# Optimization experiments

Measured on AMD Instinct MI355X. Metric: run time of the kernel, lower is better.

## Reference

```python
import jax, jax.numpy as jnp
import numpy as np

B, N, NP, NS = 8, 4096, 1024, 32
CF = 64            # input point-feature channels; in_channel = 3 + CF = 67
MLP = [64, 128, 256]
EPS = 1e-5         # BatchNorm eps (torch default)


def setup_inputs() -> dict:
    key = jax.random.key(0)
    ks = jax.random.split(key, 8)
    inp = {
        "xyz": jax.random.normal(ks[0], (B, N, 3), jnp.float32),
        "points": jax.random.normal(ks[1], (B, CF, N), jnp.float32),
        "sample_idx": jax.random.randint(ks[2], (B, NP), 0, N, dtype=jnp.int32),
        "neighbor_idx": jax.random.randint(ks[3], (B, NP, NS), 0, N, dtype=jnp.int32),
    }
    c = 3 + CF
    for i, o in enumerate(MLP):
        wk = jax.random.fold_in(ks[4], i)
        inp[f"W{i}"] = jax.random.normal(wk, (o, c), jnp.float32) * (1.0 / np.sqrt(c))
        inp[f"b{i}"] = jnp.zeros((o,), jnp.float32)
        inp[f"gamma{i}"] = jnp.ones((o,), jnp.float32)
        inp[f"beta{i}"] = jnp.zeros((o,), jnp.float32)
        c = o
    return inp


def _forward(xyz, points, sample_idx, neighbor_idx, params):
    # xyz: (B,N,3)  points: (B,CF,N)
    new_xyz = jnp.take_along_axis(xyz, sample_idx[:, :, None], axis=1)        # (B,NP,3)
    nbr_xyz = jax.vmap(lambda x, idx: x[idx])(xyz, neighbor_idx)               # (B,NP,NS,3)
    rel = nbr_xyz - new_xyz[:, :, None, :]                                     # (B,NP,NS,3)
    nbr_feat = jax.vmap(lambda f, idx: f[:, idx])(points, neighbor_idx)        # (B,CF,NP,NS)
    x = jnp.concatenate([rel.transpose(0, 3, 1, 2), nbr_feat], axis=1)         # (B,3+CF,NP,NS)
    # 1x1 Conv2d -> BatchNorm2d (training-mode batch stats) -> ReLU stack
    for W, b, g, be in params:
        x = jnp.einsum('oc,bcps->bops', W, x) + b[None, :, None, None]
        mu = x.mean(axis=(0, 2, 3), keepdims=True)
        var = x.var(axis=(0, 2, 3), keepdims=True)
        x = g[None, :, None, None] * (x - mu) * jax.lax.rsqrt(var + EPS) + be[None, :, None, None]
        x = jax.nn.relu(x)
    new_points = x.max(axis=-1)                                                # (B,C_out,NP)
    return new_xyz, new_points


def reference(xyz, points, sample_idx, neighbor_idx,
              W0, b0, gamma0, beta0,
              W1, b1, gamma1, beta1,
              W2, b2, gamma2, beta2):
    params = [(W0, b0, gamma0, beta0), (W1, b1, gamma1, beta1), (W2, b2, gamma2, beta2)]
    return _forward(xyz, points, sample_idx, neighbor_idx, params)
```

## Files before the change

### kernel.cpp

```cpp
#include <hip/hip_runtime.h>

typedef unsigned short u16;
typedef unsigned int u32;
typedef __attribute__((ext_vector_type(8))) short short8;
typedef __attribute__((ext_vector_type(16))) float f32x16;

#define BB 8
#define NN 4096
#define NPP 1024
#define NSS 32
#define CFF 64
#define C0 67
#define H0 64
#define H1 128
#define H2 256
#define MTOT (BB*NPP*NSS)
#define BN_EPS 1e-5f
#define INV_M (1.0f/262144.0f)

#define MFMA32(a,b,c) __builtin_amdgcn_mfma_f32_32x32x16_bf16(a,b,c,0,0,0)

__device__ __forceinline__ float bf2f(u16 h){ return __uint_as_float(((u32)h)<<16); }
__device__ __forceinline__ u16 f2bf(float f){
  u32 u = __float_as_uint(f);
  u32 r = (u + 0x7fffu + ((u>>16)&1u)) >> 16;
  return (u16)r;
}
__device__ __forceinline__ u32 pack2(float a, float b){
  return (u32)f2bf(a) | ((u32)f2bf(b)<<16);
}

#define WS_NEED 46280704u

__global__ __launch_bounds__(256) void k_setup(
    const float* __restrict__ xyz, const float* __restrict__ points,
    const int* __restrict__ sidx,
    const float* __restrict__ W0, const float* __restrict__ W1, const float* __restrict__ W2,
    u16* __restrict__ ptsT, u16* __restrict__ Wt0c, u16* __restrict__ Wt1c,
    u16* __restrict__ Wt2c, float* __restrict__ out_newxyz, float* __restrict__ stats)
{
  int blk = blockIdx.x, tid = threadIdx.x;
  if (blk < 512) {
    __shared__ float t[64][68];
    int b = blk >> 6, n0 = (blk & 63) << 6;
    for (int it = 0; it < 4; ++it) {
      int u = it*256 + tid;
      int nq = u & 15, c = u >> 4;
      float4 v = *(const float4*)&points[(size_t)(b*CFF + c)*NN + n0 + nq*4];
      *(float4*)&t[c][nq*4] = v;
    }
    __syncthreads();
    for (int it = 0; it < 2; ++it) {
      int u = it*256 + tid;
      int oct = u & 7, n = u >> 3;
      u16 pk[8];
#pragma unroll
      for (int j = 0; j < 8; ++j) pk[j] = f2bf(t[oct*8 + j][n]);
      *(uint4*)&ptsT[((size_t)(b*NN + n0 + n))*CFF + oct*8] = *(uint4*)pk;
    }
  } else if (blk < 544) {
    int t0 = (blk - 512)*256 + tid;
    int b = t0 >> 10;
    int s = sidx[t0];
    for (int k = 0; k < 3; ++k)
      out_newxyz[(size_t)t0*3 + k] = xyz[((size_t)(b*NN + s))*3 + k];
  } else if (blk == 544) {
    for (int i = 0; i < 24; ++i) {
      int e = i*256 + tid;
      int kc = e >> 9, o = (e >> 3) & 63, j = e & 7, k = kc*8 + j;
      float v = (k < 64) ? W0[o*C0 + 3 + k] : ((k < 67) ? W0[o*C0 + (k - 64)] : 0.f);
      Wt0c[e] = f2bf(v);
    }
  } else if (blk == 545) {
    for (int i = 0; i < 32; ++i) {
      int e = i*256 + tid;
      int kc = e >> 10, n = (e >> 3) & 127, j = e & 7;
      Wt1c[e] = f2bf(W1[n*H0 + kc*8 + j]);
    }
  } else if (blk == 554) {
    float4 z = {0.f, 0.f, 0.f, 0.f};
    float4* p = (float4*)stats;
#pragma unroll
    for (int i = 0; i < 12; ++i) p[i*256 + tid] = z;
  } else {
    int base = (blk - 546) * 4096;
    for (int i = 0; i < 16; ++i) {
      int e = base + i*256 + tid;
      int kc = e >> 11, n = (e >> 3) & 255, j = e & 7;
      Wt2c[e] = f2bf(W2[n*H1 + kc*8 + j]);
    }
  }
}

__global__ __launch_bounds__(256) void k_xyz_only(
    const float* __restrict__ xyz, const int* __restrict__ sidx, float* __restrict__ out_newxyz)
{
  int t0 = blockIdx.x*256 + threadIdx.x;
  int b = t0 >> 10;
  int s = sidx[t0];
  for (int k = 0; k < 3; ++k)
    out_newxyz[(size_t)t0*3 + k] = xyz[((size_t)(b*NN + s))*3 + k];
}

__global__ __launch_bounds__(256) void k_l0(
    const float* __restrict__ xyz, const int* __restrict__ sidx, const int* __restrict__ nidx,
    const u16* __restrict__ ptsT, const u16* __restrict__ Wt0c,
    u16* __restrict__ y0, float* __restrict__ stats)
{
  __shared__ u16 XLc[12*128*8];
  __shared__ u16 W0c[12*64*8];
  int tid = threadIdx.x;
  int m0 = blockIdx.x * 128;
  int b = m0 >> 15;

  for (int i = 0; i < 3; ++i)
    ((uint4*)W0c)[i*256 + tid] = ((const uint4*)Wt0c)[i*256 + tid];

  int pos = tid & 127, half = tid >> 7;
  int m = m0 + pos;
  int nb = nidx[m];
  {
    const uint4* prow = (const uint4*)(ptsT + ((size_t)(b*NN + nb))*CFF + half*32);
    uint4 h0 = prow[0], h1 = prow[1], h2 = prow[2], h3 = prow[3];
    *(uint4*)&XLc[((half*4+0)*128 + pos)*8] = h0;
    *(uint4*)&XLc[((half*4+1)*128 + pos)*8] = h1;
    *(uint4*)&XLc[((half*4+2)*128 + pos)*8] = h2;
    *(uint4*)&XLc[((half*4+3)*128 + pos)*8] = h3;
    if (half == 0) {
      int p = (m & 32767) >> 5;
      int sp = sidx[b*NPP + p];
      float r0 = xyz[((size_t)(b*NN+nb))*3+0] - xyz[((size_t)(b*NN+sp))*3+0];
      float r1 = xyz[((size_t)(b*NN+nb))*3+1] - xyz[((size_t)(b*NN+sp))*3+1];
      float r2 = xyz[((size_t)(b*NN+nb))*3+2] - xyz[((size_t)(b*NN+sp))*3+2];
      uint4 v = { pack2(r0, r1), pack2(r2, 0.f), 0u, 0u };
      *(uint4*)&XLc[(8*128 + pos)*8] = v;
    } else {
      uint4 z = {0u,0u,0u,0u};
      *(uint4*)&XLc[(9*128 + pos)*8]  = z;
      *(uint4*)&XLc[(10*128 + pos)*8] = z;
      *(uint4*)&XLc[(11*128 + pos)*8] = z;
    }
  }
  __syncthreads();

  int lane = tid & 63, wv = tid >> 6;
  int l31 = lane & 31, kh = lane >> 5;
  int nt = wv & 1, mtb = (wv >> 1) * 2;
  f32x16 acc[2];
  for (int mi = 0; mi < 2; ++mi) for (int r = 0; r < 16; ++r) acc[mi][r] = 0.f;

  for (int kt = 0; kt < 6; ++kt) {
    int ck = kt*2 + kh;
    short8 bfrag = *(const short8*)&W0c[(ck*64 + nt*32 + l31)*8];
    for (int mi = 0; mi < 2; ++mi) {
      short8 afrag = *(const short8*)&XLc[(ck*128 + (mtb+mi)*32 + l31)*8];
      acc[mi] = MFMA32(afrag, bfrag, acc[mi]);
    }
  }

  float s = 0.f, q = 0.f;
  for (int mi = 0; mi < 2; ++mi)
    for (int r = 0; r < 16; ++r) { float y = acc[mi][r]; s += y; q += y*y; }
  s += __shfl_xor(s, 32); q += __shfl_xor(q, 32);
  if (lane < 32) {
    int slot = blockIdx.x & 7;
    atomicAdd(&stats[slot*256 + nt*32 + lane], s);
    atomicAdd(&stats[2048 + slot*256 + nt*32 + lane], q);
  }

  __syncthreads();
  {
    int chx = (nt*32 + l31) ^ (kh*32);
#pragma unroll
    for (int mi = 0; mi < 2; ++mi)
#pragma unroll
      for (int r = 0; r < 16; ++r) {
        int mm = (mtb+mi)*32 + (r&3) + 8*(r>>2) + 4*kh;
        XLc[mm*64 + chx] = f2bf(acc[mi][r]);
      }
  }
  __syncthreads();
  {
    uint4* dst = (uint4*)(y0 + (size_t)m0*H0);
#pragma unroll
    for (int i = 0; i < 4; ++i) {
      int t16 = i*256 + tid;
      int mrow = t16 >> 3, ch0 = (t16 & 7)*8;
      int idx = mrow*64 + (ch0 ^ (32*((mrow>>2)&1)));
      dst[t16] = *(const uint4*)&XLc[idx];
    }
  }
}

__global__ __launch_bounds__(256, 4) void k_l1s(
    const u16* __restrict__ y0, const u16* __restrict__ Wt1c,
    const float* __restrict__ g0, const float* __restrict__ e0,
    const float* __restrict__ stIn, float* __restrict__ stOut)
{
  __shared__ u16 X0c[8*128*8];
  __shared__ float scl0[64], sft0[64];
  int tid = threadIdx.x;
  int m0 = blockIdx.x * 128;
  int lane = tid & 63, wv = tid >> 6;
  int l31 = lane & 31, kh = lane >> 5;

  int pos = tid & 127, half = tid >> 7;
  u16 hs[32];
  {
    const u16* row = y0 + (size_t)(m0 + pos)*H0 + half*32;
#pragma unroll
    for (int t = 0; t < 4; ++t) *(uint4*)&hs[t*8] = ((const uint4*)row)[t];
  }
  short8 b1[4];
#pragma unroll
  for (int kt = 0; kt < 4; ++kt)
    b1[kt] = *(const short8*)&Wt1c[((kt*2 + kh)*128 + wv*32 + l31)*8];

  if (tid < 64) {
    float s = 0.f, q = 0.f;
    for (int sl = 0; sl < 8; ++sl) { s += stIn[sl*256 + tid]; q += stIn[2048 + sl*256 + tid]; }
    float mu = s*INV_M, var = q*INV_M - mu*mu;
    float sc = g0[tid] * rsqrtf(var + BN_EPS);
    scl0[tid] = sc; sft0[tid] = e0[tid] - mu*sc;
  }
  __syncthreads();

  {
    u16 ob[32];
#pragma unroll
    for (int j = 0; j < 32; ++j) {
      int c = half*32 + j;
      ob[j] = f2bf(fmaxf(fmaf(scl0[c], bf2f(hs[j]), sft0[c]), 0.f));
    }
#pragma unroll
    for (int t = 0; t < 4; ++t)
      *(uint4*)&X0c[((half*4+t)*128 + pos)*8] = *(uint4*)&ob[t*8];
  }
  __syncthreads();

  f32x16 acc[4];
#pragma unroll
  for (int mt = 0; mt < 4; ++mt) for (int r = 0; r < 16; ++r) acc[mt][r] = 0.f;

#pragma unroll
  for (int kt = 0; kt < 4; ++kt) {
    int ck = kt*2 + kh;
#pragma unroll
    for (int mt = 0; mt < 4; ++mt) {
      short8 afrag = *(const short8*)&X0c[(ck*128 + mt*32 + l31)*8];
      acc[mt] = MFMA32(afrag, b1[kt], acc[mt]);
    }
  }

  float s = 0.f, q = 0.f;
#pragma unroll
  for (int mt = 0; mt < 4; ++mt)
#pragma unroll
    for (int r = 0; r < 16; ++r) { float y = acc[mt][r]; s += y; q += y*y; }
  s += __shfl_xor(s, 32); q += __shfl_xor(q, 32);
  if (lane < 32) {
    int slot = blockIdx.x & 7;
    atomicAdd(&stOut[slot*256 + wv*32 + lane], s);
    atomicAdd(&stOut[2048 + slot*256 + wv*32 + lane], q);
  }
}

__global__ __launch_bounds__(256, 4) void k_l2f(
    const u16* __restrict__ y0, const u16* __restrict__ Wt1c, const u16* __restrict__ Wt2c,
    const float* __restrict__ g0, const float* __restrict__ e0,
    const float* __restrict__ g1, const float* __restrict__ e1,
    const float* __restrict__ st0, const float* __restrict__ st1, float* __restrict__ stOut,
    u16* __restrict__ mxp, u16* __restrict__ mnp)
{
  __shared__ u16 X0c[8*64*8];
  __shared__ u16 X1c[16*64*8];
  __shared__ float scl0[64], sft0[64], scl1[128], sft1[128];
  int tid = threadIdx.x;
  int m0 = blockIdx.x * 64;
  int lane = tid & 63, wv = tid >> 6;
  int l31 = lane & 31, kh = lane >> 5;

  int pos = tid & 63, grp = tid >> 6;
  u16 hs[16];
  {
    const u16* row = y0 + (size_t)(m0 + pos)*H0 + grp*16;
    *(uint4*)&hs[0] = ((const uint4*)row)[0];
    *(uint4*)&hs[8] = ((const uint4*)row)[1];
  }
  short8 b1[4];
#pragma unroll
  for (int kt = 0; kt < 4; ++kt)
    b1[kt] = *(const short8*)&Wt1c[((kt*2 + kh)*128 + wv*32 + l31)*8];

  if (tid < 64) {
    float s = 0.f, q = 0.f;
    for (int sl = 0; sl < 8; ++sl) { s += st0[sl*256 + tid]; q += st0[2048 + sl*256 + tid]; }
    float mu = s*INV_M, var = q*INV_M - mu*mu;
    float sc = g0[tid] * rsqrtf(var + BN_EPS);
    scl0[tid] = sc; sft0[tid] = e0[tid] - mu*sc;
  }
  if (tid < 128) {
    float s = 0.f, q = 0.f;
    for (int sl = 0; sl < 8; ++sl) { s += st1[sl*256 + tid]; q += st1[2048 + sl*256 + tid]; }
    float mu = s*INV_M, var = q*INV_M - mu*mu;
    float sc = g1[tid] * rsqrtf(var + BN_EPS);
    scl1[tid] = sc; sft1[tid] = e1[tid] - mu*sc;
  }
  __syncthreads();

  {
    u16 ob[16];
#pragma unroll
    for (int j = 0; j < 16; ++j) {
      int c = grp*16 + j;
      ob[j] = f2bf(fmaxf(fmaf(scl0[c], bf2f(hs[j]), sft0[c]), 0.f));
    }
    *(uint4*)&X0c[((2*grp)*64 + pos)*8]   = *(uint4*)&ob[0];
    *(uint4*)&X0c[((2*grp+1)*64 + pos)*8] = *(uint4*)&ob[8];
  }
  __syncthreads();

  f32x16 acc1[2];
#pragma unroll
  for (int mt = 0; mt < 2; ++mt) for (int r = 0; r < 16; ++r) acc1[mt][r] = 0.f;
#pragma unroll
  for (int kt = 0; kt < 4; ++kt) {
    int ck = kt*2 + kh;
#pragma unroll
    for (int mt = 0; mt < 2; ++mt) {
      short8 afrag = *(const short8*)&X0c[(ck*64 + mt*32 + l31)*8];
      acc1[mt] = MFMA32(afrag, b1[kt], acc1[mt]);
    }
  }

  {
    int ch1 = wv*32 + l31;
    int cb = ch1 >> 3, cr = ch1 & 7, sw = cb & 3;
    float sc1 = scl1[ch1], sf1 = sft1[ch1];
#pragma unroll
    for (int mt = 0; mt < 2; ++mt)
#pragma unroll
      for (int r = 0; r < 16; ++r) {
        int mm = mt*32 + (r&3) + 8*(r>>2) + 4*kh;
        X1c[(cb*64 + (mm ^ sw))*8 + cr] = f2bf(fmaxf(fmaf(sc1, acc1[mt][r], sf1), 0.f));
      }
  }
  __syncthreads();

  f32x16 acc2[2][2];
#pragma unroll
  for (int nt = 0; nt < 2; ++nt) for (int mt = 0; mt < 2; ++mt)
    for (int r = 0; r < 16; ++r) acc2[nt][mt][r] = 0.f;

#pragma unroll
  for (int k4 = 0; k4 < 8; ++k4) {
    int ck = k4*2 + kh;
    int sw = ck & 3;
    short8 bf_[2];
#pragma unroll
    for (int nt = 0; nt < 2; ++nt)
      bf_[nt] = *(const short8*)&Wt2c[(ck*256 + wv*64 + nt*32 + l31)*8];
    short8 a[2];
#pragma unroll
    for (int mt = 0; mt < 2; ++mt)
      a[mt] = *(const short8*)&X1c[(ck*64 + ((mt*32 + l31) ^ sw))*8];
#pragma unroll
    for (int nt = 0; nt < 2; ++nt)
#pragma unroll
      for (int mt = 0; mt < 2; ++mt)
        acc2[nt][mt] = MFMA32(a[mt], bf_[nt], acc2[nt][mt]);
  }

  int slot = blockIdx.x & 7;
#pragma unroll
  for (int nt = 0; nt < 2; ++nt) {
    float s = 0.f, q = 0.f;
    float mx[2] = {-3.0e38f, -3.0e38f}, mn[2] = {3.0e38f, 3.0e38f};
#pragma unroll
    for (int mt = 0; mt < 2; ++mt)
#pragma unroll
      for (int r = 0; r < 16; ++r) {
        float y = acc2[nt][mt][r];
        s += y; q += y*y;
        mx[mt] = fmaxf(mx[mt], y); mn[mt] = fminf(mn[mt], y);
      }
    s += __shfl_xor(s, 32); q += __shfl_xor(q, 32);
    mx[0] = fmaxf(mx[0], __shfl_xor(mx[0], 32));
    mx[1] = fmaxf(mx[1], __shfl_xor(mx[1], 32));
    mn[0] = fminf(mn[0], __shfl_xor(mn[0], 32));
    mn[1] = fminf(mn[1], __shfl_xor(mn[1], 32));
    if (lane < 32) {
      int c = wv*64 + nt*32 + lane;
      atomicAdd(&stOut[slot*256 + c], s);
      atomicAdd(&stOut[2048 + slot*256 + c], q);
#pragma unroll
      for (int mt = 0; mt < 2; ++mt) {
        size_t pr = (size_t)blockIdx.x*2 + mt;
        mxp[pr*H2 + c] = f2bf(mx[mt]);
        mnp[pr*H2 + c] = f2bf(mn[mt]);
      }
    }
  }
}

__global__ __launch_bounds__(256) void k_final(
    const u16* __restrict__ mxp, const u16* __restrict__ mnp,
    const float* __restrict__ gma, const float* __restrict__ bta,
    const float* __restrict__ stIn, float* __restrict__ out_np)
{
  __shared__ float tmp[256][33];
  int tid = threadIdx.x;
  int b = blockIdx.x >> 5;
  int p0 = (blockIdx.x & 31) * 32;

  float s = 0.f, q = 0.f;
  for (int sl = 0; sl < 8; ++sl) { s += stIn[sl*256 + tid]; q += stIn[2048 + sl*256 + tid]; }
  float mu = s*INV_M, var = q*INV_M - mu*mu;
  float sc = gma[tid] * rsqrtf(var + BN_EPS);
  float sh = bta[tid] - mu*sc;

  for (int pp = 0; pp < 32; ++pp) {
    size_t base = ((size_t)(b*NPP + p0 + pp))*H2 + tid;
    float xv = bf2f(mxp[base]), nv = bf2f(mnp[base]);
    float v = (sc >= 0.f) ? fmaf(sc, xv, sh) : fmaf(sc, nv, sh);
    tmp[tid][pp] = fmaxf(v, 0.f);
  }
  __syncthreads();

  int pl = tid & 31, cg = tid >> 5;
  for (int cc = 0; cc < 32; ++cc) {
    int c = cc*8 + cg;
    out_np[((size_t)b*H2 + c)*NPP + p0 + pl] = tmp[c][pl];
  }
}

extern "C" void kernel_launch(void* const* d_in, const int* in_sizes, int n_in,
                              void* d_out, int out_size, void* d_ws, size_t ws_size,
                              hipStream_t stream)
{
  const float* xyz    = (const float*)d_in[0];
  const float* points = (const float*)d_in[1];
  const int*   sidx   = (const int*)d_in[2];
  const int*   nidx   = (const int*)d_in[3];
  const float* W0 = (const float*)d_in[4];
  const float* g0 = (const float*)d_in[6];
  const float* e0 = (const float*)d_in[7];
  const float* W1 = (const float*)d_in[8];
  const float* g1 = (const float*)d_in[10];
  const float* e1 = (const float*)d_in[11];
  const float* W2 = (const float*)d_in[12];
  const float* g2 = (const float*)d_in[14];
  const float* e2 = (const float*)d_in[15];

  float* out_xyz = (float*)d_out;
  float* out_np  = out_xyz + (size_t)BB*NPP*3;

  if (ws_size < (size_t)WS_NEED) {
    hipMemsetAsync(out_np, 0, (size_t)BB*H2*NPP*4, stream);
    k_xyz_only<<<32, 256, 0, stream>>>(xyz, sidx, out_xyz);
    return;
  }

  char* ws = (char*)d_ws;
  float* stats = (float*)(ws + 0);
  u16*   Wt0c  = (u16*)(ws + 49152);
  u16*   Wt1c  = (u16*)(ws + 61440);
  u16*   Wt2c  = (u16*)(ws + 77824);
  u16*   ptsT  = (u16*)(ws + 143360);
  u16*   y0    = (u16*)(ws + 4337664);
  u16*   mxp   = (u16*)(ws + 37892096);
  u16*   mnp   = (u16*)(ws + 42086400);

  k_setup<<<555, 256, 0, stream>>>(xyz, points, sidx, W0, W1, W2,
                                   ptsT, Wt0c, Wt1c, Wt2c, out_xyz, stats);
  k_l0<<<MTOT/128, 256, 0, stream>>>(xyz, sidx, nidx, ptsT, Wt0c, y0, stats);
  k_l1s<<<MTOT/128, 256, 0, stream>>>(y0, Wt1c, g0, e0, stats, stats + 4096);
  k_l2f<<<MTOT/64, 256, 0, stream>>>(y0, Wt1c, Wt2c, g0, e0, g1, e1,
                                     stats, stats + 4096, stats + 8192, mxp, mnp);
  k_final<<<256, 256, 0, stream>>>(mxp, mnp, g2, e2, stats + 8192, out_np);
}
```

Before: 166.8 us.

## Fuse all stages into one persistent kernel with software grid barriers

Replaces the five separate launches (setup, layer0, layer1 stats, layer2 fused, final) with a single persistent kernel of 512 blocks that loops over tiles and uses atomic-counter grid barriers between phases. A tiny init kernel clears the barrier counters. This removes per-launch overhead and inter-kernel gaps. The risk is that it relies on all 512 blocks being co-resident, that the barriers' spinning and fences add cost, and that the fixed grid may lower occupancy compared with launching thousands of blocks per stage.

```diff
diff --git a/kernel.cpp b/kernel.cpp
--- a/kernel.cpp
+++ b/kernel.cpp
@@ -17,6 +17,7 @@
 #define MTOT (BB*NPP*NSS)
 #define BN_EPS 1e-5f
 #define INV_M (1.0f/262144.0f)
+#define NBLK 512
 
 #define MFMA32(a,b,c) __builtin_amdgcn_mfma_f32_32x32x16_bf16(a,b,c,0,0,0)
 
@@ -30,66 +31,30 @@
   return (u32)f2bf(a) | ((u32)f2bf(b)<<16);
 }
 
-#define WS_NEED 46280704u
-
-__global__ __launch_bounds__(256) void k_setup(
-    const float* __restrict__ xyz, const float* __restrict__ points,
-    const int* __restrict__ sidx,
-    const float* __restrict__ W0, const float* __restrict__ W1, const float* __restrict__ W2,
-    u16* __restrict__ ptsT, u16* __restrict__ Wt0c, u16* __restrict__ Wt1c,
-    u16* __restrict__ Wt2c, float* __restrict__ out_newxyz, float* __restrict__ stats)
+#define WS_NEED 46281728u
+
+__device__ __forceinline__ void gbar(char* bar, int idx) {
+  __syncthreads();
+  if (threadIdx.x == 0) {
+    __threadfence();
+    int* cnt = (int*)(bar + idx*256);
+    int* gen = (int*)(bar + idx*256 + 128);
+    if (__hip_atomic_fetch_add(cnt, 1, __ATOMIC_ACQ_REL, __HIP_MEMORY_SCOPE_AGENT) == NBLK - 1) {
+      __hip_atomic_store(gen, 1, __ATOMIC_RELEASE, __HIP_MEMORY_SCOPE_AGENT);
+    } else {
+      int spins = 0;
+      while (__hip_atomic_load(gen, __ATOMIC_ACQUIRE, __HIP_MEMORY_SCOPE_AGENT) == 0) {
+        if (++spins > (1 << 24)) break;
+      }
+    }
+    __threadfence();
+  }
+  __syncthreads();
+}
+
+__global__ __launch_bounds__(256) void k_binit(char* __restrict__ bar)
 {
-  int blk = blockIdx.x, tid = threadIdx.x;
-  if (blk < 512) {
-    __shared__ float t[64][68];
-    int b = blk >> 6, n0 = (blk & 63) << 6;
-    for (int it = 0; it < 4; ++it) {
-      int u = it*256 + tid;
-      int nq = u & 15, c = u >> 4;
-      float4 v = *(const float4*)&points[(size_t)(b*CFF + c)*NN + n0 + nq*4];
-      *(float4*)&t[c][nq*4] = v;
-    }
-    __syncthreads();
-    for (int it = 0; it < 2; ++it) {
-      int u = it*256 + tid;
-      int oct = u & 7, n = u >> 3;
-      u16 pk[8];
-#pragma unroll
-      for (int j = 0; j < 8; ++j) pk[j] = f2bf(t[oct*8 + j][n]);
-      *(uint4*)&ptsT[((size_t)(b*NN + n0 + n))*CFF + oct*8] = *(uint4*)pk;
-    }
-  } else if (blk < 544) {
-    int t0 = (blk - 512)*256 + tid;
-    int b = t0 >> 10;
-    int s = sidx[t0];
-    for (int k = 0; k < 3; ++k)
-      out_newxyz[(size_t)t0*3 + k] = xyz[((size_t)(b*NN + s))*3 + k];
-  } else if (blk == 544) {
-    for (int i = 0; i < 24; ++i) {
-      int e = i*256 + tid;
-      int kc = e >> 9, o = (e >> 3) & 63, j = e & 7, k = kc*8 + j;
-      float v = (k < 64) ? W0[o*C0 + 3 + k] : ((k < 67) ? W0[o*C0 + (k - 64)] : 0.f);
-      Wt0c[e] = f2bf(v);
-    }
-  } else if (blk == 545) {
-    for (int i = 0; i < 32; ++i) {
-      int e = i*256 + tid;
-      int kc = e >> 10, n = (e >> 3) & 127, j = e & 7;
-      Wt1c[e] = f2bf(W1[n*H0 + kc*8 + j]);
-    }
-  } else if (blk == 554) {
-    float4 z = {0.f, 0.f, 0.f, 0.f};
-    float4* p = (float4*)stats;
-#pragma unroll
-    for (int i = 0; i < 12; ++i) p[i*256 + tid] = z;
-  } else {
-    int base = (blk - 546) * 4096;
-    for (int i = 0; i < 16; ++i) {
-      int e = base + i*256 + tid;
-      int kc = e >> 11, n = (e >> 3) & 255, j = e & 7;
-      Wt2c[e] = f2bf(W2[n*H1 + kc*8 + j]);
-    }
-  }
+  if (threadIdx.x < 256) ((int*)bar)[threadIdx.x] = 0;
 }
 
 __global__ __launch_bounds__(256) void k_xyz_only(
@@ -102,335 +67,406 @@
     out_newxyz[(size_t)t0*3 + k] = xyz[((size_t)(b*NN + s))*3 + k];
 }
 
-__global__ __launch_bounds__(256) void k_l0(
-    const float* __restrict__ xyz, const int* __restrict__ sidx, const int* __restrict__ nidx,
-    const u16* __restrict__ ptsT, const u16* __restrict__ Wt0c,
-    u16* __restrict__ y0, float* __restrict__ stats)
+__global__ __launch_bounds__(256, 4) void k_all(
+    const float* __restrict__ xyz, const float* __restrict__ points,
+    const int* __restrict__ sidx, const int* __restrict__ nidx,
+    const float* __restrict__ W0, const float* __restrict__ g0, const float* __restrict__ e0,
+    const float* __restrict__ W1, const float* __restrict__ g1, const float* __restrict__ e1,
+    const float* __restrict__ W2, const float* __restrict__ g2, const float* __restrict__ e2,
+    char* __restrict__ ws, float* __restrict__ out_xyz)
 {
-  __shared__ u16 XLc[12*128*8];
-  __shared__ u16 W0c[12*64*8];
-  int tid = threadIdx.x;
-  int m0 = blockIdx.x * 128;
-  int b = m0 >> 15;
-
-  for (int i = 0; i < 3; ++i)
-    ((uint4*)W0c)[i*256 + tid] = ((const uint4*)Wt0c)[i*256 + tid];
-
-  int pos = tid & 127, half = tid >> 7;
-  int m = m0 + pos;
-  int nb = nidx[m];
+  __shared__ __align__(16) unsigned char smem[36864];
+  float* stats = (float*)ws;
+  u16* Wt0c = (u16*)(ws + 49152);
+  u16* Wt1c = (u16*)(ws + 61440);
+  u16* Wt2c = (u16*)(ws + 77824);
+  u16* ptsT = (u16*)(ws + 143360);
+  u16* y0   = (u16*)(ws + 4337664);
+  u16* mxp  = (u16*)(ws + 37892096);
+  u16* mnp  = (u16*)(ws + 42086400);
+  char* bar = ws + 46280704;
+  float* out_np = out_xyz + (size_t)BB*NPP*3;
+
+  int bid = blockIdx.x, tid = threadIdx.x;
+
+  for (int u = bid; u < 555; u += NBLK) {
+    if (u < 512) {
+      float (*t)[68] = (float(*)[68])smem;
+      int b = u >> 6, n0 = (u & 63) << 6;
+      for (int it = 0; it < 4; ++it) {
+        int e = it*256 + tid;
+        int nq = e & 15, c = e >> 4;
+        float4 v = *(const float4*)&points[(size_t)(b*CFF + c)*NN + n0 + nq*4];
+        *(float4*)&t[c][nq*4] = v;
+      }
+      __syncthreads();
+      for (int it = 0; it < 2; ++it) {
+        int e = it*256 + tid;
+        int oct = e & 7, n = e >> 3;
+        u16 pk[8];
+#pragma unroll
+        for (int j = 0; j < 8; ++j) pk[j] = f2bf(t[oct*8 + j][n]);
+        *(uint4*)&ptsT[((size_t)(b*NN + n0 + n))*CFF + oct*8] = *(uint4*)pk;
+      }
+      __syncthreads();
+    } else if (u < 544) {
+      int t0 = (u - 512)*256 + tid;
+      int b = t0 >> 10;
+      int s = sidx[t0];
+      for (int k = 0; k < 3; ++k)
+        out_xyz[(size_t)t0*3 + k] = xyz[((size_t)(b*NN + s))*3 + k];
+    } else if (u == 544) {
+      for (int i = 0; i < 24; ++i) {
+        int e = i*256 + tid;
+        int kc = e >> 9, o = (e >> 3) & 63, j = e & 7, k = kc*8 + j;
+        float v = (k < 64) ? W0[o*C0 + 3 + k] : ((k < 67) ? W0[o*C0 + (k - 64)] : 0.f);
+        Wt0c[e] = f2bf(v);
+      }
+    } else if (u == 545) {
+      for (int i = 0; i < 32; ++i) {
+        int e = i*256 + tid;
+        int kc = e >> 10, n = (e >> 3) & 127, j = e & 7;
+        Wt1c[e] = f2bf(W1[n*H0 + kc*8 + j]);
+      }
+    } else if (u == 554) {
+      float4 z = {0.f, 0.f, 0.f, 0.f};
+      float4* p = (float4*)stats;
+#pragma unroll
+      for (int i = 0; i < 12; ++i) p[i*256 + tid] = z;
+    } else {
+      int base = (u - 546) * 4096;
+      for (int i = 0; i < 16; ++i) {
+        int e = base + i*256 + tid;
+        int kc = e >> 11, n = (e >> 3) & 255, j = e & 7;
+        Wt2c[e] = f2bf(W2[n*H1 + kc*8 + j]);
+      }
+    }
+  }
+  gbar(bar, 0);
+
   {
-    const uint4* prow = (const uint4*)(ptsT + ((size_t)(b*NN + nb))*CFF + half*32);
-    uint4 h0 = prow[0], h1 = prow[1], h2 = prow[2], h3 = prow[3];
-    *(uint4*)&XLc[((half*4+0)*128 + pos)*8] = h0;
-    *(uint4*)&XLc[((half*4+1)*128 + pos)*8] = h1;
-    *(uint4*)&XLc[((half*4+2)*128 + pos)*8] = h2;
-    *(uint4*)&XLc[((half*4+3)*128 + pos)*8] = h3;
-    if (half == 0) {
-      int p = (m & 32767) >> 5;
-      int sp = sidx[b*NPP + p];
-      float r0 = xyz[((size_t)(b*NN+nb))*3+0] - xyz[((size_t)(b*NN+sp))*3+0];
-      float r1 = xyz[((size_t)(b*NN+nb))*3+1] - xyz[((size_t)(b*NN+sp))*3+1];
-      float r2 = xyz[((size_t)(b*NN+nb))*3+2] - xyz[((size_t)(b*NN+sp))*3+2];
-      uint4 v = { pack2(r0, r1), pack2(r2, 0.f), 0u, 0u };
-      *(uint4*)&XLc[(8*128 + pos)*8] = v;
-    } else {
-      uint4 z = {0u,0u,0u,0u};
-      *(uint4*)&XLc[(9*128 + pos)*8]  = z;
-      *(uint4*)&XLc[(10*128 + pos)*8] = z;
-      *(uint4*)&XLc[(11*128 + pos)*8] = z;
-    }
-  }
-  __syncthreads();
-
-  int lane = tid & 63, wv = tid >> 6;
-  int l31 = lane & 31, kh = lane >> 5;
-  int nt = wv & 1, mtb = (wv >> 1) * 2;
-  f32x16 acc[2];
-  for (int mi = 0; mi < 2; ++mi) for (int r = 0; r < 16; ++r) acc[mi][r] = 0.f;
-
-  for (int kt = 0; kt < 6; ++kt) {
-    int ck = kt*2 + kh;
-    short8 bfrag = *(const short8*)&W0c[(ck*64 + nt*32 + l31)*8];
-    for (int mi = 0; mi < 2; ++mi) {
-      short8 afrag = *(const short8*)&XLc[(ck*128 + (mtb+mi)*32 + l31)*8];
-      acc[mi] = MFMA32(afrag, bfrag, acc[mi]);
-    }
-  }
-
-  float s = 0.f, q = 0.f;
-  for (int mi = 0; mi < 2; ++mi)
-    for (int r = 0; r < 16; ++r) { float y = acc[mi][r]; s += y; q += y*y; }
-  s += __shfl_xor(s, 32); q += __shfl_xor(q, 32);
-  if (lane < 32) {
-    int slot = blockIdx.x & 7;
-    atomicAdd(&stats[slot*256 + nt*32 + lane], s);
-    atomicAdd(&stats[2048 + slot*256 + nt*32 + lane], q);
-  }
-
-  __syncthreads();
+    u16* XLc = (u16*)smem;
+    u16* W0c = (u16*)(smem + 24576);
+    for (int i = 0; i < 3; ++i)
+      ((uint4*)W0c)[i*256 + tid] = ((const uint4*)Wt0c)[i*256 + tid];
+
+    int pos = tid & 127, half = tid >> 7;
+    int lane = tid & 63, wv = tid >> 6;
+    int l31 = lane & 31, kh = lane >> 5;
+    int nt = wv & 1, mtb = (wv >> 1) * 2;
+
+    for (int tile = bid; tile < 2048; tile += NBLK) {
+      int m0 = tile * 128;
+      int b = m0 >> 15;
+      int m = m0 + pos;
+      int nb = nidx[m];
+
+      __syncthreads();
+      {
+        const uint4* prow = (const uint4*)(ptsT + ((size_t)(b*NN + nb))*CFF + half*32);
+        uint4 h0 = prow[0], h1 = prow[1], h2 = prow[2], h3 = prow[3];
+        *(uint4*)&XLc[((half*4+0)*128 + pos)*8] = h0;
+        *(uint4*)&XLc[((half*4+1)*128 + pos)*8] = h1;
+        *(uint4*)&XLc[((half*4+2)*128 + pos)*8] = h2;
+        *(uint4*)&XLc[((half*4+3)*128 + pos)*8] = h3;
+        if (half == 0) {
+          int p = (m & 32767) >> 5;
+          int sp = sidx[b*NPP + p];
+          float r0 = xyz[((size_t)(b*NN+nb))*3+0] - xyz[((size_t)(b*NN+sp))*3+0];
+          float r1 = xyz[((size_t)(b*NN+nb))*3+1] - xyz[((size_t)(b*NN+sp))*3+1];
+          float r2 = xyz[((size_t)(b*NN+nb))*3+2] - xyz[((size_t)(b*NN+sp))*3+2];
+          uint4 v = { pack2(r0, r1), pack2(r2, 0.f), 0u, 0u };
+          *(uint4*)&XLc[(8*128 + pos)*8] = v;
+        } else {
+          uint4 z = {0u,0u,0u,0u};
+          *(uint4*)&XLc[(9*128 + pos)*8]  = z;
+          *(uint4*)&XLc[(10*128 + pos)*8] = z;
+          *(uint4*)&XLc[(11*128 + pos)*8] = z;
+        }
+      }
+      __syncthreads();
+
+      f32x16 acc[2];
+#pragma unroll
+      for (int mi = 0; mi < 2; ++mi) for (int r = 0; r < 16; ++r) acc[mi][r] = 0.f;
+#pragma unroll
+      for (int kt = 0; kt < 6; ++kt) {
+        int ck = kt*2 + kh;
+        short8 bfrag = *(const short8*)&W0c[(ck*64 + nt*32 + l31)*8];
+#pragma unroll
+        for (int mi = 0; mi < 2; ++mi) {
+          short8 afrag = *(const short8*)&XLc[(ck*128 + (mtb+mi)*32 + l31)*8];
+          acc[mi] = MFMA32(afrag, bfrag, acc[mi]);
+        }
+      }
+
+      float s = 0.f, q = 0.f;
+#pragma unroll
+      for (int mi = 0; mi < 2; ++mi)
+#pragma unroll
+        for (int r = 0; r < 16; ++r) { float y = acc[mi][r]; s += y; q += y*y; }
+      s += __shfl_xor(s, 32); q += __shfl_xor(q, 32);
+      if (lane < 32) {
+        int slot = tile & 7;
+        atomicAdd(&stats[slot*256 + nt*32 + lane], s);
+        atomicAdd(&stats[2048 + slot*256 + nt*32 + lane], q);
+      }
+
+      __syncthreads();
+      {
+        int chx = (nt*32 + l31) ^ (kh*32);
+#pragma unroll
+        for (int mi = 0; mi < 2; ++mi)
+#pragma unroll
+          for (int r = 0; r < 16; ++r) {
+            int mm = (mtb+mi)*32 + (r&3) + 8*(r>>2) + 4*kh;
+            XLc[mm*64 + chx] = f2bf(acc[mi][r]);
+          }
+      }
+      __syncthreads();
+      {
+        uint4* dst = (uint4*)(y0 + (size_t)m0*H0);
+#pragma unroll
+        for (int i = 0; i < 4; ++i) {
+          int t16 = i*256 + tid;
+          int mrow = t16 >> 3, ch0 = (t16 & 7)*8;
+          int idx = mrow*64 + (ch0 ^ (32*((mrow>>2)&1)));
+          dst[t16] = *(const uint4*)&XLc[idx];
+        }
+      }
+    }
+  }
+  gbar(bar, 1);
+
   {
-    int chx = (nt*32 + l31) ^ (kh*32);
-#pragma unroll
-    for (int mi = 0; mi < 2; ++mi)
-#pragma unroll
-      for (int r = 0; r < 16; ++r) {
-        int mm = (mtb+mi)*32 + (r&3) + 8*(r>>2) + 4*kh;
-        XLc[mm*64 + chx] = f2bf(acc[mi][r]);
-      }
-  }
-  __syncthreads();
+    u16* X0c = (u16*)smem;
+    float* scl0 = (float*)(smem + 16384);
+    float* sft0 = (float*)(smem + 16640);
+    if (tid < 64) {
+      float s = 0.f, q = 0.f;
+      for (int sl = 0; sl < 8; ++sl) { s += stats[sl*256 + tid]; q += stats[2048 + sl*256 + tid]; }
+      float mu = s*INV_M, var = q*INV_M - mu*mu;
+      float sc = g0[tid] * rsqrtf(var + BN_EPS);
+      scl0[tid] = sc; sft0[tid] = e0[tid] - mu*sc;
+    }
+    int lane = tid & 63, wv = tid >> 6;
+    int l31 = lane & 31, kh = lane >> 5;
+    int pos = tid & 127, half = tid >> 7;
+
+    for (int tile = bid; tile < 2048; tile += NBLK) {
+      int m0 = tile * 128;
+      u16 hs[32];
+      {
+        const u16* row = y0 + (size_t)(m0 + pos)*H0 + half*32;
+#pragma unroll
+        for (int t = 0; t < 4; ++t) *(uint4*)&hs[t*8] = ((const uint4*)row)[t];
+      }
+      short8 b1[4];
+#pragma unroll
+      for (int kt = 0; kt < 4; ++kt)
+        b1[kt] = *(const short8*)&Wt1c[((kt*2 + kh)*128 + wv*32 + l31)*8];
+
+      __syncthreads();
+      {
+        u16 ob[32];
+#pragma unroll
+        for (int j = 0; j < 32; ++j) {
+          int c = half*32 + j;
+          ob[j] = f2bf(fmaxf(fmaf(scl0[c], bf2f(hs[j]), sft0[c]), 0.f));
+        }
+#pragma unroll
+        for (int t = 0; t < 4; ++t)
+          *(uint4*)&X0c[((half*4+t)*128 + pos)*8] = *(uint4*)&ob[t*8];
+      }
+      __syncthreads();
+
+      f32x16 acc[4];
+#pragma unroll
+      for (int mt = 0; mt < 4; ++mt) for (int r = 0; r < 16; ++r) acc[mt][r] = 0.f;
+#pragma unroll
+      for (int kt = 0; kt < 4; ++kt) {
+        int ck = kt*2 + kh;
+#pragma unroll
+        for (int mt = 0; mt < 4; ++mt) {
+          short8 afrag = *(const short8*)&X0c[(ck*128 + mt*32 + l31)*8];
+          acc[mt] = MFMA32(afrag, b1[kt], acc[mt]);
+        }
+      }
+
+      float s = 0.f, q = 0.f;
+#pragma unroll
+      for (int mt = 0; mt < 4; ++mt)
+#pragma unroll
+        for (int r = 0; r < 16; ++r) { float y = acc[mt][r]; s += y; q += y*y; }
+      s += __shfl_xor(s, 32); q += __shfl_xor(q, 32);
+      if (lane < 32) {
+        int slot = tile & 7;
+        atomicAdd(&stats[4096 + slot*256 + wv*32 + lane], s);
+        atomicAdd(&stats[4096 + 2048 + slot*256 + wv*32 + lane], q);
+      }
+    }
+  }
+  gbar(bar, 2);
+
   {
-    uint4* dst = (uint4*)(y0 + (size_t)m0*H0);
-#pragma unroll
-    for (int i = 0; i < 4; ++i) {
-      int t16 = i*256 + tid;
-      int mrow = t16 >> 3, ch0 = (t16 & 7)*8;
-      int idx = mrow*64 + (ch0 ^ (32*((mrow>>2)&1)));
-      dst[t16] = *(const uint4*)&XLc[idx];
-    }
-  }
-}
-
-__global__ __launch_bounds__(256, 4) void k_l1s(
-    const u16* __restrict__ y0, const u16* __restrict__ Wt1c,
-    const float* __restrict__ g0, const float* __restrict__ e0,
-    const float* __restrict__ stIn, float* __restrict__ stOut)
-{
-  __shared__ u16 X0c[8*128*8];
-  __shared__ float scl0[64], sft0[64];
-  int tid = threadIdx.x;
-  int m0 = blockIdx.x * 128;
-  int lane = tid & 63, wv = tid >> 6;
-  int l31 = lane & 31, kh = lane >> 5;
-
-  int pos = tid & 127, half = tid >> 7;
-  u16 hs[32];
-  {
-    const u16* row = y0 + (size_t)(m0 + pos)*H0 + half*32;
-#pragma unroll
-    for (int t = 0; t < 4; ++t) *(uint4*)&hs[t*8] = ((const uint4*)row)[t];
-  }
-  short8 b1[4];
-#pragma unroll
-  for (int kt = 0; kt < 4; ++kt)
-    b1[kt] = *(const short8*)&Wt1c[((kt*2 + kh)*128 + wv*32 + l31)*8];
-
-  if (tid < 64) {
+    u16* X0c = (u16*)smem;
+    u16* X1c = (u16*)(smem + 8192);
+    float* scl0 = (float*)(smem + 24576);
+    float* sft0 = (float*)(smem + 24832);
+    float* scl1 = (float*)(smem + 25088);
+    float* sft1 = (float*)(smem + 25600);
+    if (tid < 64) {
+      float s = 0.f, q = 0.f;
+      for (int sl = 0; sl < 8; ++sl) { s += stats[sl*256 + tid]; q += stats[2048 + sl*256 + tid]; }
+      float mu = s*INV_M, var = q*INV_M - mu*mu;
+      float sc = g0[tid] * rsqrtf(var + BN_EPS);
+      scl0[tid] = sc; sft0[tid] = e0[tid] - mu*sc;
+    }
+    if (tid < 128) {
+      float s = 0.f, q = 0.f;
+      for (int sl = 0; sl < 8; ++sl) { s += stats[4096 + sl*256 + tid]; q += stats[4096 + 2048 + sl*256 + tid]; }
+      float mu = s*INV_M, var = q*INV_M - mu*mu;
+      float sc = g1[tid] * rsqrtf(var + BN_EPS);
+      scl1[tid] = sc; sft1[tid] = e1[tid] - mu*sc;
+    }
+    int lane = tid & 63, wv = tid >> 6;
+    int l31 = lane & 31, kh = lane >> 5;
+    int pos = tid & 63, grp = tid >> 6;
+
+    for (int tile = bid; tile < 4096; tile += NBLK) {
+      int m0 = tile * 64;
+      u16 hs[16];
+      {
+        const u16* row = y0 + (size_t)(m0 + pos)*H0 + grp*16;
+        *(uint4*)&hs[0] = ((const uint4*)row)[0];
+        *(uint4*)&hs[8] = ((const uint4*)row)[1];
+      }
+      short8 b1[4];
+#pragma unroll
+      for (int kt = 0; kt < 4; ++kt)
+        b1[kt] = *(const short8*)&Wt1c[((kt*2 + kh)*128 + wv*32 + l31)*8];
+
+      __syncthreads();
+      {
+        u16 ob[16];
+#pragma unroll
+        for (int j = 0; j < 16; ++j) {
+          int c = grp*16 + j;
+          ob[j] = f2bf(fmaxf(fmaf(scl0[c], bf2f(hs[j]), sft0[c]), 0.f));
+        }
+        *(uint4*)&X0c[((2*grp)*64 + pos)*8]   = *(uint4*)&ob[0];
+        *(uint4*)&X0c[((2*grp+1)*64 + pos)*8] = *(uint4*)&ob[8];
+      }
+      __syncthreads();
+
+      f32x16 acc1[2];
+#pragma unroll
+      for (int mt = 0; mt < 2; ++mt) for (int r = 0; r < 16; ++r) acc1[mt][r] = 0.f;
+#pragma unroll
+      for (int kt = 0; kt < 4; ++kt) {
+        int ck = kt*2 + kh;
+#pragma unroll
+        for (int mt = 0; mt < 2; ++mt) {
+          short8 afrag = *(const short8*)&X0c[(ck*64 + mt*32 + l31)*8];
+          acc1[mt] = MFMA32(afrag, b1[kt], acc1[mt]);
+        }
+      }
+
+      {
+        int ch1 = wv*32 + l31;
+        int cb = ch1 >> 3, cr = ch1 & 7, sw = cb & 3;
+        float sc1 = scl1[ch1], sf1 = sft1[ch1];
+#pragma unroll
+        for (int mt = 0; mt < 2; ++mt)
+#pragma unroll
+          for (int r = 0; r < 16; ++r) {
+            int mm = mt*32 + (r&3) + 8*(r>>2) + 4*kh;
+            X1c[(cb*64 + (mm ^ sw))*8 + cr] = f2bf(fmaxf(fmaf(sc1, acc1[mt][r], sf1), 0.f));
+          }
+      }
+      __syncthreads();
+
+      f32x16 acc2[2][2];
+#pragma unroll
+      for (int nt = 0; nt < 2; ++nt) for (int mt = 0; mt < 2; ++mt)
+        for (int r = 0; r < 16; ++r) acc2[nt][mt][r] = 0.f;
+#pragma unroll
+      for (int k4 = 0; k4 < 8; ++k4) {
+        int ck = k4*2 + kh;
+        int sw = ck & 3;
+        short8 bf_[2];
+#pragma unroll
+        for (int nt = 0; nt < 2; ++nt)
+          bf_[nt] = *(const short8*)&Wt2c[(ck*256 + wv*64 + nt*32 + l31)*8];
+        short8 a[2];
+#pragma unroll
+        for (int mt = 0; mt < 2; ++mt)
+          a[mt] = *(const short8*)&X1c[(ck*64 + ((mt*32 + l31) ^ sw))*8];
+#pragma unroll
+        for (int nt = 0; nt < 2; ++nt)
+#pragma unroll
+          for (int mt = 0; mt < 2; ++mt)
+            acc2[nt][mt] = MFMA32(a[mt], bf_[nt], acc2[nt][mt]);
+      }
+
+      int slot = tile & 7;
+#pragma unroll
+      for (int nt = 0; nt < 2; ++nt) {
+        float s = 0.f, q = 0.f;
+        float mx[2] = {-3.0e38f, -3.0e38f}, mn[2] = {3.0e38f, 3.0e38f};
+#pragma unroll
+        for (int mt = 0; mt < 2; ++mt)
+#pragma unroll
+          for (int r = 0; r < 16; ++r) {
+            float y = acc2[nt][mt][r];
+            s += y; q += y*y;
+            mx[mt] = fmaxf(mx[mt], y); mn[mt] = fminf(mn[mt], y);
+          }
+        s += __shfl_xor(s, 32); q += __shfl_xor(q, 32);
+        mx[0] = fmaxf(mx[0], __shfl_xor(mx[0], 32));
+        mx[1] = fmaxf(mx[1], __shfl_xor(mx[1], 32));
+        mn[0] = fminf(mn[0], __shfl_xor(mn[0], 32));
+        mn[1] = fminf(mn[1], __shfl_xor(mn[1], 32));
+        if (lane < 32) {
+          int c = wv*64 + nt*32 + lane;
+          atomicAdd(&stats[8192 + slot*256 + c], s);
+          atomicAdd(&stats[8192 + 2048 + slot*256 + c], q);
+#pragma unroll
+          for (int mt = 0; mt < 2; ++mt) {
+            size_t pr = (size_t)tile*2 + mt;
+            mxp[pr*H2 + c] = f2bf(mx[mt]);
+            mnp[pr*H2 + c] = f2bf(mn[mt]);
+          }
+        }
+      }
+    }
+  }
+  gbar(bar, 3);
+
+  if (bid < 256) {
+    float (*tmp)[33] = (float(*)[33])smem;
+    int b = bid >> 5;
+    int p0 = (bid & 31) * 32;
+
     float s = 0.f, q = 0.f;
-    for (int sl = 0; sl < 8; ++sl) { s += stIn[sl*256 + tid]; q += stIn[2048 + sl*256 + tid]; }
+    for (int sl = 0; sl < 8; ++sl) { s += stats[8192 + sl*256 + tid]; q += stats[8192 + 2048 + sl*256 + tid]; }
     float mu = s*INV_M, var = q*INV_M - mu*mu;
-    float sc = g0[tid] * rsqrtf(var + BN_EPS);
-    scl0[tid] = sc; sft0[tid] = e0[tid] - mu*sc;
-  }
-  __syncthreads();
-
-  {
-    u16 ob[32];
-#pragma unroll
-    for (int j = 0; j < 32; ++j) {
-      int c = half*32 + j;
-      ob[j] = f2bf(fmaxf(fmaf(scl0[c], bf2f(hs[j]), sft0[c]), 0.f));
-    }
-#pragma unroll
-    for (int t = 0; t < 4; ++t)
-      *(uint4*)&X0c[((half*4+t)*128 + pos)*8] = *(uint4*)&ob[t*8];
-  }
-  __syncthreads();
-
-  f32x16 acc[4];
-#pragma unroll
-  for (int mt = 0; mt < 4; ++mt) for (int r = 0; r < 16; ++r) acc[mt][r] = 0.f;
-
-#pragma unroll
-  for (int kt = 0; kt < 4; ++kt) {
-    int ck = kt*2 + kh;
-#pragma unroll
-    for (int mt = 0; mt < 4; ++mt) {
-      short8 afrag = *(const short8*)&X0c[(ck*128 + mt*32 + l31)*8];
-      acc[mt] = MFMA32(afrag, b1[kt], acc[mt]);
-    }
-  }
-
-  float s = 0.f, q = 0.f;
-#pragma unroll
-  for (int mt = 0; mt < 4; ++mt)
-#pragma unroll
-    for (int r = 0; r < 16; ++r) { float y = acc[mt][r]; s += y; q += y*y; }
-  s += __shfl_xor(s, 32); q += __shfl_xor(q, 32);
-  if (lane < 32) {
-    int slot = blockIdx.x & 7;
-    atomicAdd(&stOut[slot*256 + wv*32 + lane], s);
-    atomicAdd(&stOut[2048 + slot*256 + wv*32 + lane], q);
-  }
-}
-
-__global__ __launch_bounds__(256, 4) void k_l2f(
-    const u16* __restrict__ y0, const u16* __restrict__ Wt1c, const u16* __restrict__ Wt2c,
-    const float* __restrict__ g0, const float* __restrict__ e0,
-    const float* __restrict__ g1, const float* __restrict__ e1,
-    const float* __restrict__ st0, const float* __restrict__ st1, float* __restrict__ stOut,
-    u16* __restrict__ mxp, u16* __restrict__ mnp)
-{
-  __shared__ u16 X0c[8*64*8];
-  __shared__ u16 X1c[16*64*8];
-  __shared__ float scl0[64], sft0[64], scl1[128], sft1[128];
-  int tid = threadIdx.x;
-  int m0 = blockIdx.x * 64;
-  int lane = tid & 63, wv = tid >> 6;
-  int l31 = lane & 31, kh = lane >> 5;
-
-  int pos = tid & 63, grp = tid >> 6;
-  u16 hs[16];
-  {
-    const u16* row = y0 + (size_t)(m0 + pos)*H0 + grp*16;
-    *(uint4*)&hs[0] = ((const uint4*)row)[0];
-    *(uint4*)&hs[8] = ((const uint4*)row)[1];
-  }
-  short8 b1[4];
-#pragma unroll
-  for (int kt = 0; kt < 4; ++kt)
-    b1[kt] = *(const short8*)&Wt1c[((kt*2 + kh)*128 + wv*32 + l31)*8];
-
-  if (tid < 64) {
-    float s = 0.f, q = 0.f;
-    for (int sl = 0; sl < 8; ++sl) { s += st0[sl*256 + tid]; q += st0[2048 + sl*256 + tid]; }
-    float mu = s*INV_M, var = q*INV_M - mu*mu;
-    float sc = g0[tid] * rsqrtf(var + BN_EPS);
-    scl0[tid] = sc; sft0[tid] = e0[tid] - mu*sc;
-  }
-  if (tid < 128) {
-    float s = 0.f, q = 0.f;
-    for (int sl = 0; sl < 8; ++sl) { s += st1[sl*256 + tid]; q += st1[2048 + sl*256 + tid]; }
-    float mu = s*INV_M, var = q*INV_M - mu*mu;
-    float sc = g1[tid] * rsqrtf(var + BN_EPS);
-    scl1[tid] = sc; sft1[tid] = e1[tid] - mu*sc;
-  }
-  __syncthreads();
-
-  {
-    u16 ob[16];
-#pragma unroll
-    for (int j = 0; j < 16; ++j) {
-      int c = grp*16 + j;
-      ob[j] = f2bf(fmaxf(fmaf(scl0[c], bf2f(hs[j]), sft0[c]), 0.f));
-    }
-    *(uint4*)&X0c[((2*grp)*64 + pos)*8]   = *(uint4*)&ob[0];
-    *(uint4*)&X0c[((2*grp+1)*64 + pos)*8] = *(uint4*)&ob[8];
-  }
-  __syncthreads();
-
-  f32x16 acc1[2];
-#pragma unroll
-  for (int mt = 0; mt < 2; ++mt) for (int r = 0; r < 16; ++r) acc1[mt][r] = 0.f;
-#pragma unroll
-  for (int kt = 0; kt < 4; ++kt) {
-    int ck = kt*2 + kh;
-#pragma unroll
-    for (int mt = 0; mt < 2; ++mt) {
-      short8 afrag = *(const short8*)&X0c[(ck*64 + mt*32 + l31)*8];
-      acc1[mt] = MFMA32(afrag, b1[kt], acc1[mt]);
-    }
-  }
-
-  {
-    int ch1 = wv*32 + l31;
-    int cb = ch1 >> 3, cr = ch1 & 7, sw = cb & 3;
-    float sc1 = scl1[ch1], sf1 = sft1[ch1];
-#pragma unroll
-    for (int mt = 0; mt < 2; ++mt)
-#pragma unroll
-      for (int r = 0; r < 16; ++r) {
-        int mm = mt*32 + (r&3) + 8*(r>>2) + 4*kh;
-        X1c[(cb*64 + (mm ^ sw))*8 + cr] = f2bf(fmaxf(fmaf(sc1, acc1[mt][r], sf1), 0.f));
-      }
-  }
-  __syncthreads();
-
-  f32x16 acc2[2][2];
-#pragma unroll
-  for (int nt = 0; nt < 2; ++nt) for (int mt = 0; mt < 2; ++mt)
-    for (int r = 0; r < 16; ++r) acc2[nt][mt][r] = 0.f;
-
-#pragma unroll
-  for (int k4 = 0; k4 < 8; ++k4) {
-    int ck = k4*2 + kh;
-    int sw = ck & 3;
-    short8 bf_[2];
-#pragma unroll
-    for (int nt = 0; nt < 2; ++nt)
-      bf_[nt] = *(const short8*)&Wt2c[(ck*256 + wv*64 + nt*32 + l31)*8];
-    short8 a[2];
-#pragma unroll
-    for (int mt = 0; mt < 2; ++mt)
-      a[mt] = *(const short8*)&X1c[(ck*64 + ((mt*32 + l31) ^ sw))*8];
-#pragma unroll
-    for (int nt = 0; nt < 2; ++nt)
-#pragma unroll
-      for (int mt = 0; mt < 2; ++mt)
-        acc2[nt][mt] = MFMA32(a[mt], bf_[nt], acc2[nt][mt]);
-  }
-
-  int slot = blockIdx.x & 7;
-#pragma unroll
-  for (int nt = 0; nt < 2; ++nt) {
-    float s = 0.f, q = 0.f;
-    float mx[2] = {-3.0e38f, -3.0e38f}, mn[2] = {3.0e38f, 3.0e38f};
-#pragma unroll
-    for (int mt = 0; mt < 2; ++mt)
-#pragma unroll
-      for (int r = 0; r < 16; ++r) {
-        float y = acc2[nt][mt][r];
-        s += y; q += y*y;
-        mx[mt] = fmaxf(mx[mt], y); mn[mt] = fminf(mn[mt], y);
-      }
-    s += __shfl_xor(s, 32); q += __shfl_xor(q, 32);
-    mx[0] = fmaxf(mx[0], __shfl_xor(mx[0], 32));
-    mx[1] = fmaxf(mx[1], __shfl_xor(mx[1], 32));
-    mn[0] = fminf(mn[0], __shfl_xor(mn[0], 32));
-    mn[1] = fminf(mn[1], __shfl_xor(mn[1], 32));
-    if (lane < 32) {
-      int c = wv*64 + nt*32 + lane;
-      atomicAdd(&stOut[slot*256 + c], s);
-      atomicAdd(&stOut[2048 + slot*256 + c], q);
-#pragma unroll
-      for (int mt = 0; mt < 2; ++mt) {
-        size_t pr = (size_t)blockIdx.x*2 + mt;
-        mxp[pr*H2 + c] = f2bf(mx[mt]);
-        mnp[pr*H2 + c] = f2bf(mn[mt]);
-      }
-    }
-  }
-}
-
-__global__ __launch_bounds__(256) void k_final(
-    const u16* __restrict__ mxp, const u16* __restrict__ mnp,
-    const float* __restrict__ gma, const float* __restrict__ bta,
-    const float* __restrict__ stIn, float* __restrict__ out_np)
-{
-  __shared__ float tmp[256][33];
-  int tid = threadIdx.x;
-  int b = blockIdx.x >> 5;
-  int p0 = (blockIdx.x & 31) * 32;
-
-  float s = 0.f, q = 0.f;
-  for (int sl = 0; sl < 8; ++sl) { s += stIn[sl*256 + tid]; q += stIn[2048 + sl*256 + tid]; }
-  float mu = s*INV_M, var = q*INV_M - mu*mu;
-  float sc = gma[tid] * rsqrtf(var + BN_EPS);
-  float sh = bta[tid] - mu*sc;
-
-  for (int pp = 0; pp < 32; ++pp) {
-    size_t base = ((size_t)(b*NPP + p0 + pp))*H2 + tid;
-    float xv = bf2f(mxp[base]), nv = bf2f(mnp[base]);
-    float v = (sc >= 0.f) ? fmaf(sc, xv, sh) : fmaf(sc, nv, sh);
-    tmp[tid][pp] = fmaxf(v, 0.f);
-  }
-  __syncthreads();
-
-  int pl = tid & 31, cg = tid >> 5;
-  for (int cc = 0; cc < 32; ++cc) {
-    int c = cc*8 + cg;
-    out_np[((size_t)b*H2 + c)*NPP + p0 + pl] = tmp[c][pl];
+    float sc = g2[tid] * rsqrtf(var + BN_EPS);
+    float sh = e2[tid] - mu*sc;
+
+    for (int pp = 0; pp < 32; ++pp) {
+      size_t base = ((size_t)(b*NPP + p0 + pp))*H2 + tid;
+      float xv = bf2f(mxp[base]), nv = bf2f(mnp[base]);
+      float v = (sc >= 0.f) ? fmaf(sc, xv, sh) : fmaf(sc, nv, sh);
+      tmp[tid][pp] = fmaxf(v, 0.f);
+    }
+    __syncthreads();
+
+    int pl = tid & 31, cg2 = tid >> 5;
+    for (int cc = 0; cc < 32; ++cc) {
+      int c = cc*8 + cg2;
+      out_np[((size_t)b*H2 + c)*NPP + p0 + pl] = tmp[c][pl];
+    }
   }
 }
 
@@ -462,20 +498,8 @@
   }
 
   char* ws = (char*)d_ws;
-  float* stats = (float*)(ws + 0);
-  u16*   Wt0c  = (u16*)(ws + 49152);
-  u16*   Wt1c  = (u16*)(ws + 61440);
-  u16*   Wt2c  = (u16*)(ws + 77824);
-  u16*   ptsT  = (u16*)(ws + 143360);
-  u16*   y0    = (u16*)(ws + 4337664);
-  u16*   mxp   = (u16*)(ws + 37892096);
-  u16*   mnp   = (u16*)(ws + 42086400);
-
-  k_setup<<<555, 256, 0, stream>>>(xyz, points, sidx, W0, W1, W2,
-                                   ptsT, Wt0c, Wt1c, Wt2c, out_xyz, stats);
-  k_l0<<<MTOT/128, 256, 0, stream>>>(xyz, sidx, nidx, ptsT, Wt0c, y0, stats);
-  k_l1s<<<MTOT/128, 256, 0, stream>>>(y0, Wt1c, g0, e0, stats, stats + 4096);
-  k_l2f<<<MTOT/64, 256, 0, stream>>>(y0, Wt1c, Wt2c, g0, e0, g1, e1,
-                                     stats, stats + 4096, stats + 8192, mxp, mnp);
-  k_final<<<256, 256, 0, stream>>>(mxp, mnp, g2, e2, stats + 8192, out_np);
-}
+  k_binit<<<1, 256, 0, stream>>>(ws + 46280704);
+  k_all<<<NBLK, 256, 0, stream>>>(xyz, points, sidx, nidx,
+                                  W0, g0, e0, W1, g1, e1, W2, g2, e2,
+                                  ws, out_xyz);
+}
```

After: 456.1 us. 173% more time.
